# Kernel optimization log

Measured on AMD Instinct MI355X. Metric: run time of the kernel, lower is better.

## Reference

```python
import jax, jax.numpy as jnp
import numpy as np

B = 16384          # batch of graphs
N = 4              # nodes per graph (hardcoded in module)
F_IN = 4           # node features
F_E = 4            # edge features
CH = 128           # EdgeConditionedConv channels
HID = 256          # final Dense units (gnn hidden_dim)
OBS_DIM = 3 + N * F_IN + N * N + N * N * F_E  # 99


def _glorot(k, shape, fan):
    return jax.random.normal(k, shape, jnp.float32) * (1.0 / np.sqrt(fan))


def setup_inputs() -> dict:
    key = jax.random.key(0)
    ks = jax.random.split(key, 8)
    return {
        "observations": jax.random.normal(ks[0], (B, OBS_DIM), jnp.float32),
        # ECCConv filter-generating network: single Dense(F_E -> CH*F_IN)
        "W_fgn": _glorot(ks[1], (F_E, CH * F_IN), F_E),
        "b_fgn": jnp.zeros((CH * F_IN,), jnp.float32),
        # ECCConv root weight + bias
        "W_root": _glorot(ks[2], (F_IN, CH), F_IN),
        "b_conv": jnp.zeros((CH,), jnp.float32),
        # GlobalAttnSumPool attention vector
        "attn_kernel": _glorot(ks[3], (CH,), CH),
        # final Dense(tanh)
        "W_dense": _glorot(ks[4], (CH, HID), CH),
        "b_dense": jnp.zeros((HID,), jnp.float32),
    }


def reference(observations, W_fgn, b_fgn, W_root, b_conv, attn_kernel, W_dense, b_dense):
    Bn = observations.shape[0]
    obs = observations[:, 3:]
    X = obs[:, : N * F_IN].reshape(Bn, N, F_IN)                     # [B,N,F]
    A = obs[:, N * F_IN : N * F_IN + N * N].reshape(Bn, N, N)        # [B,N,N]
    E = obs[:, N * F_IN + N * N :].reshape(Bn, N, N, F_E)            # [B,N,N,Fe]

    # EdgeConditionedConv: per-edge filter generated from edge features,
    # reshaped to (B, N, N, CH, F_IN)  [channels-out first, as in spektral]
    K = (E @ W_fgn + b_fgn).reshape(Bn, N, N, CH, F_IN)
    # out[b,t,c] = sum_{s,f} A[b,t,s] * K[b,t,s,c,f] * X[b,s,f]  + root + bias
    msg = jnp.einsum('btscf,bts,bsf->btc', K, A, X)
    Xc = jax.nn.relu(msg + X @ W_root + b_conv)                      # [B,N,CH]

    # GlobalAttnSumPool: softmax over nodes of X @ a, weighted sum
    attn = jax.nn.softmax(jnp.einsum('bnc,c->bn', Xc, attn_kernel), axis=-1)
    pooled = jnp.einsum('bn,bnc->bc', attn, Xc)                      # [B,CH]

    return jnp.tanh(pooled @ W_dense + b_dense)                      # [B,HID]
```

## Files before the change

kernel.cpp:

```cpp
#include <hip/hip_runtime.h>

#define OBS_DIM 99
#define CH      128
#define HID     256
#define BPB     16

typedef short s8v __attribute__((ext_vector_type(8)));
typedef short s4v __attribute__((ext_vector_type(4)));
typedef float f4v __attribute__((ext_vector_type(4)));

__device__ __forceinline__ float ftanh(float x) {
    const float t = __expf(2.f * x);
    return 1.f - 2.f * __builtin_amdgcn_rcpf(t + 1.f);
}

__device__ __forceinline__ unsigned short f2bf(float f) {
    union { float f; unsigned u; } v; v.f = f;
    unsigned r = (v.u + 0x7fffu + ((v.u >> 16) & 1u)) >> 16;
    return (unsigned short)r;
}

__device__ __forceinline__ float bf2f(unsigned short u) {
    union { unsigned u; float f; } v; v.u = ((unsigned)u) << 16;
    return v.f;
}

__device__ __forceinline__ int kmap(int vb, int g, int j) {
    return vb ? (g * 4 + (j & 3) + 16 * (j >> 2)) : (g * 8 + j);
}

__device__ __forceinline__ float wbig_val(int k, int c, const float* Wf,
                                          const float* bf, const float* Wr,
                                          const float* bc) {
    if (k < 16) return Wf[(k >> 2) * 512 + c * 4 + (k & 3)];
    if (k < 20) return bf[c * 4 + (k - 16)];
    if (k < 24) return Wr[(k - 20) * CH + c];
    if (k == 24) return bc[c];
    return 0.f;
}

__global__ __launch_bounds__(256) void prepack(const float* __restrict__ W,
                                               const float* __restrict__ Wf,
                                               const float* __restrict__ bf,
                                               const float* __restrict__ Wr,
                                               const float* __restrict__ bc,
                                               unsigned short* __restrict__ ws) {
    const int gid = blockIdx.x * 256 + threadIdx.x;
    if (gid < 8192) {
        const int vb = gid >> 12, g = gid & 4095;
        const int tile = g >> 6, l = g & 63;
        const int kt = tile >> 4, nt = tile & 15;
        const int h = nt * 16 + (l & 15);
        unsigned short vh[8], vl[8];
        #pragma unroll
        for (int j = 0; j < 8; ++j) {
            const int k = kt * 32 + kmap(vb, l >> 4, j);
            const float wv = W[(size_t)k * HID + h];
            vh[j] = f2bf(wv);
            vl[j] = f2bf(wv - bf2f(vh[j]));
        }
        unsigned short* dh = ws + (size_t)vb * 65536 + (size_t)g * 8;
        *reinterpret_cast<s8v*>(dh)         = *reinterpret_cast<const s8v*>(vh);
        *reinterpret_cast<s8v*>(dh + 32768) = *reinterpret_cast<const s8v*>(vl);
    } else if (gid < 9216) {
        const int g2 = gid - 8192;
        const int vb = g2 >> 9, rest = g2 & 511;
        const int nt = rest >> 6, l = rest & 63;
        const int c = nt * 16 + (l & 15);
        unsigned short vh[8], vl[8];
        #pragma unroll
        for (int j = 0; j < 8; ++j) {
            const int k = kmap(vb, l >> 4, j);
            const float wv = wbig_val(k, c, Wf, bf, Wr, bc);
            vh[j] = f2bf(wv);
            vl[j] = f2bf(wv - bf2f(vh[j]));
        }
        unsigned short* dh = ws + 131072 + (size_t)vb * 8192 + (size_t)(nt * 64 + l) * 8;
        *reinterpret_cast<s8v*>(dh)        = *reinterpret_cast<const s8v*>(vh);
        *reinterpret_cast<s8v*>(dh + 4096) = *reinterpret_cast<const s8v*>(vl);
    }
}

template <int USE_MFMA>
__global__ __launch_bounds__(256, 3) void gnn_fused(
    const float* __restrict__ obs,
    const float* __restrict__ W_fgn,
    const float* __restrict__ b_fgn,
    const float* __restrict__ W_root,
    const float* __restrict__ b_conv,
    const float* __restrict__ attn_k,
    const float* __restrict__ W_dense,
    const unsigned short* __restrict__ wb,
    const float* __restrict__ b_dense,
    float* __restrict__ out)
{
    __shared__ __align__(16) unsigned char smem[43264];
    auto feat_h  = reinterpret_cast<unsigned short (*)[40]>(smem);
    auto feat_l  = reinterpret_cast<unsigned short (*)[40]>(smem + 5120);
    auto lobs    = reinterpret_cast<float (*)[96]>(smem + 10240);
    auto xcp     = reinterpret_cast<float (*)[129]>(smem + 10240);
    auto part    = reinterpret_cast<float (*)[64]>(smem + 5120);
    auto attnl   = reinterpret_cast<float*>(smem + 6144);
    auto lpool_h = reinterpret_cast<unsigned short (*)[136]>(smem);
    auto lpool_l = reinterpret_cast<unsigned short (*)[136]>(smem + 10240);

    const int tid  = threadIdx.x;
    const int b0   = blockIdx.x * BPB;
    const int lane = tid & 63;
    const int w    = tid >> 6;

    for (int i = tid; i < BPB * 96; i += 256) {
        const int bi = i / 96, col = i - bi * 96;
        lobs[bi][col] = obs[(size_t)(b0 + bi) * OBS_DIM + 3 + col];
    }

    int variant = 3;
    int bi_r[4] = {0, 0, 0, 0}, hx_r[4] = {0, 0, 0, 0};
    if (USE_MFMA) {
        s8v ac, ab2, lab, ones;
        #pragma unroll
        for (int j = 0; j < 8; ++j) {
            const int g = lane >> 4;
            ac[j]   = (short)f2bf((float)(kmap(0, g, j) + 1));
            ab2[j]  = (short)f2bf((float)(kmap(1, g, j) + 1));
            lab[j]  = (short)f2bf((float)(lane & 15));
            ones[j] = (short)0x3F80;
        }
        const f4v z = {0.f, 0.f, 0.f, 0.f};
        const f4v dcc = __builtin_amdgcn_mfma_f32_16x16x32_bf16(ac,  ac,  z, 0, 0, 0);
        const f4v dcb = __builtin_amdgcn_mfma_f32_16x16x32_bf16(ac,  ab2, z, 0, 0, 0);
        const f4v dbc = __builtin_amdgcn_mfma_f32_16x16x32_bf16(ab2, ac,  z, 0, 0, 0);
        const float EXP = 11440.f;
        if      (__all(dcc[0] == EXP)) variant = 0;
        else if (__all(dcb[0] == EXP)) variant = 1;
        else if (__all(dbc[0] == EXP)) variant = 2;

        const f4v rowv = __builtin_amdgcn_mfma_f32_16x16x32_bf16(lab, ones, z, 0, 0, 0);
        const f4v colv = __builtin_amdgcn_mfma_f32_16x16x32_bf16(ones, lab, z, 0, 0, 0);
        #pragma unroll
        for (int r = 0; r < 4; ++r) {
            int bv = (int)(rowv[r] * 0.03125f + 0.5f);
            int hv = (int)(colv[r] * 0.03125f + 0.5f);
            bi_r[r] = bv < 0 ? 0 : (bv > 15 ? 15 : bv);
            hx_r[r] = hv < 0 ? 0 : (hv > 15 ? 15 : hv);
        }
    }
    __syncthreads();

    {
        const int bi = tid >> 4, t = (tid >> 2) & 3, e = tid & 3;
        const int row = bi * 4 + t;
        float m[4] = {0.f, 0.f, 0.f, 0.f};
        #pragma unroll
        for (int s = 0; s < 4; ++s) {
            const float ae = lobs[bi][16 + t * 4 + s] * lobs[bi][32 + (t * 4 + s) * 4 + e];
            #pragma unroll
            for (int f = 0; f < 4; ++f) m[f] = fmaf(ae, lobs[bi][s * 4 + f], m[f]);
        }
        #pragma unroll
        for (int f = 0; f < 4; ++f) {
            const unsigned short h = f2bf(m[f]);
            feat_h[row][e * 4 + f] = h;
            feat_l[row][e * 4 + f] = f2bf(m[f] - bf2f(h));
        }
    }
    if (tid < 64) {
        const int bi = tid >> 2, t = tid & 3, row = bi * 4 + t;
        #pragma unroll
        for (int f = 0; f < 4; ++f) {
            float ax = 0.f;
            #pragma unroll
            for (int s = 0; s < 4; ++s)
                ax = fmaf(lobs[bi][16 + t * 4 + s], lobs[bi][s * 4 + f], ax);
            const unsigned short h = f2bf(ax);
            feat_h[row][16 + f] = h;
            feat_l[row][16 + f] = f2bf(ax - bf2f(h));
        }
    } else if (tid < 128) {
        const int q = tid - 64;
        const int bi = q >> 2, t = q & 3, row = bi * 4 + t;
        #pragma unroll
        for (int f = 0; f < 4; ++f) {
            const float xv = lobs[bi][t * 4 + f];
            const unsigned short h = f2bf(xv);
            feat_h[row][20 + f] = h;
            feat_l[row][20 + f] = f2bf(xv - bf2f(h));
        }
        feat_h[row][24] = 0x3F80; feat_l[row][24] = 0;
        #pragma unroll
        for (int k = 25; k < 32; ++k) { feat_h[row][k] = 0; feat_l[row][k] = 0; }
    }
    __syncthreads();

    if (variant < 3) {
        const s8v* B1h = reinterpret_cast<const s8v*>(wb + 131072 + (variant == 1 ? 8192 : 0));
        const s8v* B1l = B1h + 512;
        s8v bh[2], bl[2];
        #pragma unroll
        for (int ctl = 0; ctl < 2; ++ctl) {
            const int idx = (w * 2 + ctl) * 64 + lane;
            bh[ctl] = B1h[idx]; bl[ctl] = B1l[idx];
        }
        #pragma unroll
        for (int rt = 0; rt < 4; ++rt) {
            const int row = rt * 16 + (lane & 15);
            s8v ah, al;
            if (variant != 2) {
                ah = *reinterpret_cast<const s8v*>(&feat_h[row][(lane >> 4) * 8]);
                al = *reinterpret_cast<const s8v*>(&feat_l[row][(lane >> 4) * 8]);
            } else {
                const s4v h0 = *reinterpret_cast<const s4v*>(&feat_h[row][(lane >> 4) * 4]);
                const s4v h1 = *reinterpret_cast<const s4v*>(&feat_h[row][16 + (lane >> 4) * 4]);
                const s4v l0 = *reinterpret_cast<const s4v*>(&feat_l[row][(lane >> 4) * 4]);
                const s4v l1 = *reinterpret_cast<const s4v*>(&feat_l[row][16 + (lane >> 4) * 4]);
                ah = __builtin_shufflevector(h0, h1, 0, 1, 2, 3, 4, 5, 6, 7);
                al = __builtin_shufflevector(l0, l1, 0, 1, 2, 3, 4, 5, 6, 7);
            }
            #pragma unroll
            for (int ctl = 0; ctl < 2; ++ctl) {
                f4v acc = {0.f, 0.f, 0.f, 0.f};
                acc = __builtin_amdgcn_mfma_f32_16x16x32_bf16(al, bh[ctl], acc, 0, 0, 0);
                acc = __builtin_amdgcn_mfma_f32_16x16x32_bf16(ah, bl[ctl], acc, 0, 0, 0);
                acc = __builtin_amdgcn_mfma_f32_16x16x32_bf16(ah, bh[ctl], acc, 0, 0, 0);
                const int ct = w * 2 + ctl;
                #pragma unroll
                for (int r = 0; r < 4; ++r)
                    xcp[rt * 16 + bi_r[r]][ct * 16 + hx_r[r]] = fmaxf(acc[r], 0.f);
            }
        }
    } else {
        const int c = tid & 127, hf = tid >> 7;
        for (int r = hf * 32; r < hf * 32 + 32; ++r) {
            float s = 0.f;
            #pragma unroll 5
            for (int k = 0; k < 25; ++k)
                s = fmaf(bf2f(feat_h[r][k]) + bf2f(feat_l[r][k]),
                         wbig_val(k, c, W_fgn, b_fgn, W_root, b_conv), s);
            xcp[r][c] = fmaxf(s, 0.f);
        }
    }
    __syncthreads();

    {
        const int cb = w * 32;
        float p = 0.f;
        #pragma unroll 8
        for (int cc = 0; cc < 32; ++cc)
            p = fmaf(xcp[lane][cb + cc], attn_k[cb + cc], p);
        part[w][lane] = p;
    }
    __syncthreads();

    if (tid < 64) {
        const float l = part[0][tid] + part[1][tid] + part[2][tid] + part[3][tid];
        float m1 = fmaxf(l, __shfl_xor(l, 1, 64));
        m1 = fmaxf(m1, __shfl_xor(m1, 2, 64));
        const float e = __expf(l - m1);
        float s = e + __shfl_xor(e, 1, 64);
        s += __shfl_xor(s, 2, 64);
        attnl[tid] = e * __builtin_amdgcn_rcpf(s);
    }
    __syncthreads();

    {
        const int item = tid >> 4, cb = (tid & 15) * 8;
        float pl[8] = {0.f, 0.f, 0.f, 0.f, 0.f, 0.f, 0.f, 0.f};
        #pragma unroll
        for (int t = 0; t < 4; ++t) {
            const float a = attnl[item * 4 + t];
            #pragma unroll
            for (int j = 0; j < 8; ++j)
                pl[j] = fmaf(a, xcp[item * 4 + t][cb + j], pl[j]);
        }
        __syncthreads();
        #pragma unroll
        for (int j = 0; j < 8; ++j) {
            const unsigned short h = f2bf(pl[j]);
            lpool_h[item][cb + j] = h;
            lpool_l[item][cb + j] = f2bf(pl[j] - bf2f(h));
        }
    }
    __syncthreads();

    if (variant < 3) {
        const s8v* Bh = reinterpret_cast<const s8v*>(wb + (variant == 1 ? 65536 : 0));
        const s8v* Bl = reinterpret_cast<const s8v*>(wb + (variant == 1 ? 98304 : 32768));
        f4v acc[4] = {f4v{0,0,0,0}, f4v{0,0,0,0}, f4v{0,0,0,0}, f4v{0,0,0,0}};
        #pragma unroll
        for (int ks = 0; ks < 4; ++ks) {
            s8v ah, al;
            if (variant != 2) {
                ah = *reinterpret_cast<const s8v*>(&lpool_h[lane & 15][ks * 32 + (lane >> 4) * 8]);
                al = *reinterpret_cast<const s8v*>(&lpool_l[lane & 15][ks * 32 + (lane >> 4) * 8]);
            } else {
                const s4v h0 = *reinterpret_cast<const s4v*>(&lpool_h[lane & 15][ks * 32 + (lane >> 4) * 4]);
                const s4v h1 = *reinterpret_cast<const s4v*>(&lpool_h[lane & 15][ks * 32 + 16 + (lane >> 4) * 4]);
                const s4v l0 = *reinterpret_cast<const s4v*>(&lpool_l[lane & 15][ks * 32 + (lane >> 4) * 4]);
                const s4v l1 = *reinterpret_cast<const s4v*>(&lpool_l[lane & 15][ks * 32 + 16 + (lane >> 4) * 4]);
                ah = __builtin_shufflevector(h0, h1, 0, 1, 2, 3, 4, 5, 6, 7);
                al = __builtin_shufflevector(l0, l1, 0, 1, 2, 3, 4, 5, 6, 7);
            }
            #pragma unroll
            for (int nt = 0; nt < 4; ++nt) {
                const int idx = (ks * 16 + w * 4 + nt) * 64 + lane;
                const s8v bh = Bh[idx], bl = Bl[idx];
                acc[nt] = __builtin_amdgcn_mfma_f32_16x16x32_bf16(al, bh, acc[nt], 0, 0, 0);
                acc[nt] = __builtin_amdgcn_mfma_f32_16x16x32_bf16(ah, bl, acc[nt], 0, 0, 0);
                acc[nt] = __builtin_amdgcn_mfma_f32_16x16x32_bf16(ah, bh, acc[nt], 0, 0, 0);
            }
        }
        #pragma unroll
        for (int nt = 0; nt < 4; ++nt) {
            #pragma unroll
            for (int r = 0; r < 4; ++r) {
                const int h = w * 64 + nt * 16 + hx_r[r];
                out[(size_t)(b0 + bi_r[r]) * HID + h] = ftanh(acc[nt][r] + b_dense[h]);
            }
        }
    } else {
        const int col0 = w * 64 + (lane & 15) * 4;
        const int rb   = (lane >> 4) * 4;
        float acc[4][4];
        #pragma unroll
        for (int j = 0; j < 4; ++j)
            #pragma unroll
            for (int i = 0; i < 4; ++i) acc[j][i] = 0.f;
        for (int cc = 0; cc < CH; ++cc) {
            const float4 wr = *reinterpret_cast<const float4*>(&W_dense[(size_t)cc * HID + col0]);
            #pragma unroll
            for (int j = 0; j < 4; ++j) {
                const float p = bf2f(lpool_h[rb + j][cc]) + bf2f(lpool_l[rb + j][cc]);
                acc[j][0] = fmaf(p, wr.x, acc[j][0]);
                acc[j][1] = fmaf(p, wr.y, acc[j][1]);
                acc[j][2] = fmaf(p, wr.z, acc[j][2]);
                acc[j][3] = fmaf(p, wr.w, acc[j][3]);
            }
        }
        const float4 bd = *reinterpret_cast<const float4*>(&b_dense[col0]);
        #pragma unroll
        for (int j = 0; j < 4; ++j) {
            float4 o;
            o.x = ftanh(acc[j][0] + bd.x);
            o.y = ftanh(acc[j][1] + bd.y);
            o.z = ftanh(acc[j][2] + bd.z);
            o.w = ftanh(acc[j][3] + bd.w);
            *reinterpret_cast<float4*>(&out[(size_t)(b0 + rb + j) * HID + col0]) = o;
        }
    }
}

extern "C" void kernel_launch(void* const* d_in, const int* in_sizes, int n_in,
                              void* d_out, int out_size, void* d_ws, size_t ws_size,
                              hipStream_t stream) {
    const float* obs     = (const float*)d_in[0];
    const float* W_fgn   = (const float*)d_in[1];
    const float* b_fgn   = (const float*)d_in[2];
    const float* W_root  = (const float*)d_in[3];
    const float* b_conv  = (const float*)d_in[4];
    const float* attn_k  = (const float*)d_in[5];
    const float* W_dense = (const float*)d_in[6];
    const float* b_dense = (const float*)d_in[7];
    float* out = (float*)d_out;

    const int Bn = in_sizes[0] / OBS_DIM;
    const bool use_mfma = (ws_size >= 320 * 1024) && (d_ws != nullptr);

    if (use_mfma) {
        unsigned short* wb = (unsigned short*)d_ws;
        prepack<<<36, 256, 0, stream>>>(W_dense, W_fgn, b_fgn, W_root, b_conv, wb);
        gnn_fused<1><<<Bn / BPB, 256, 0, stream>>>(obs, W_fgn, b_fgn, W_root, b_conv,
                                                   attn_k, W_dense, wb, b_dense, out);
    } else {
        gnn_fused<0><<<Bn / BPB, 256, 0, stream>>>(obs, W_fgn, b_fgn, W_root, b_conv,
                                                   attn_k, W_dense, nullptr, b_dense, out);
    }
}
```

Baseline: 27.05 us.

## Keep conv outputs in registers, fuse attention pooling, hoist MFMA layout probe to prepack

The per-block MFMA layout and variant probe moves into the prepack kernel and is written once to workspace. The main kernel reads it from there. The ECC conv outputs now stay in registers, and attention logits are reduced with shuffles instead of through a 64x129 shared-memory tile. This shrinks shared memory from about 43KB to 19KB and raises launch bounds to 4 blocks per SM for more occupancy. The cost is more register pressure from holding xc, plus a dependency on the probe result in global memory.

```diff
diff --git a/kernel.cpp b/kernel.cpp
--- a/kernel.cpp
+++ b/kernel.cpp
@@ -79,10 +79,64 @@
         *reinterpret_cast<s8v*>(dh)        = *reinterpret_cast<const s8v*>(vh);
         *reinterpret_cast<s8v*>(dh + 4096) = *reinterpret_cast<const s8v*>(vl);
     }
-}
-
-template <int USE_MFMA>
-__global__ __launch_bounds__(256, 3) void gnn_fused(
+
+    if (blockIdx.x == 0 && threadIdx.x < 64) {
+        const int lane = threadIdx.x;
+        const int g = lane >> 4;
+        s8v ac, ab2, lab, ones;
+        #pragma unroll
+        for (int j = 0; j < 8; ++j) {
+            ac[j]   = (short)f2bf((float)(kmap(0, g, j) + 1));
+            ab2[j]  = (short)f2bf((float)(kmap(1, g, j) + 1));
+            lab[j]  = (short)f2bf((float)(lane & 15));
+            ones[j] = (short)0x3F80;
+        }
+        const f4v z = {0.f, 0.f, 0.f, 0.f};
+        const f4v dcc = __builtin_amdgcn_mfma_f32_16x16x32_bf16(ac,  ac,  z, 0, 0, 0);
+        const f4v dcb = __builtin_amdgcn_mfma_f32_16x16x32_bf16(ac,  ab2, z, 0, 0, 0);
+        const f4v dbc = __builtin_amdgcn_mfma_f32_16x16x32_bf16(ab2, ac,  z, 0, 0, 0);
+        const float EXP = 11440.f;
+        int variant = 3;
+        if      (__all(dcc[0] == EXP)) variant = 0;
+        else if (__all(dcb[0] == EXP)) variant = 1;
+        else if (__all(dbc[0] == EXP)) variant = 2;
+
+        const f4v rowv = __builtin_amdgcn_mfma_f32_16x16x32_bf16(lab, ones, z, 0, 0, 0);
+        const f4v colv = __builtin_amdgcn_mfma_f32_16x16x32_bf16(ones, lab, z, 0, 0, 0);
+        int bi[4], hx[4];
+        #pragma unroll
+        for (int r = 0; r < 4; ++r) {
+            int bv = (int)(rowv[r] * 0.03125f + 0.5f);
+            int hv = (int)(colv[r] * 0.03125f + 0.5f);
+            bi[r] = bv < 0 ? 0 : (bv > 15 ? 15 : bv);
+            hx[r] = hv < 0 ? 0 : (hv > 15 ? 15 : hv);
+        }
+        bool gb = (bi[0] >> 2 == bi[1] >> 2) && (bi[1] >> 2 == bi[2] >> 2) &&
+                  (bi[2] >> 2 == bi[3] >> 2);
+        gb = gb && (((1 << (bi[0] & 3)) | (1 << (bi[1] & 3)) |
+                     (1 << (bi[2] & 3)) | (1 << (bi[3] & 3))) == 0xF);
+        gb = gb && (hx[0] == hx[1]) && (hx[1] == hx[2]) && (hx[2] == hx[3]);
+        const int pk = bi[0] | (bi[1] << 4) | (bi[2] << 8) | (bi[3] << 12)
+                     | (hx[0] << 16) | (hx[1] << 20) | (hx[2] << 24) | (hx[3] << 28);
+        int bip = pk & 0xFFFF;
+        bool same = true;
+        #pragma unroll
+        for (int st = 1; st < 16; st <<= 1)
+            same = same && (bip == __shfl_xor(bip, st, 64));
+        unsigned mset = 1u << hx[0];
+        #pragma unroll
+        for (int st = 1; st < 16; st <<= 1)
+            mset |= (unsigned)__shfl_xor((int)mset, st, 64);
+        gb = gb && same && (mset == 0xFFFFu);
+        const int gb_all = __all(gb ? 1 : 0);
+
+        int* pr = reinterpret_cast<int*>(ws + 147456);
+        pr[lane] = pk;
+        if (lane == 0) pr[64] = variant | (gb_all ? 16 : 0);
+    }
+}
+
+__global__ __launch_bounds__(256, 4) void gnn_main(
     const float* __restrict__ obs,
     const float* __restrict__ W_fgn,
     const float* __restrict__ b_fgn,
@@ -91,59 +145,42 @@
     const float* __restrict__ attn_k,
     const float* __restrict__ W_dense,
     const unsigned short* __restrict__ wb,
+    const int* __restrict__ probe,
     const float* __restrict__ b_dense,
     float* __restrict__ out)
 {
-    __shared__ __align__(16) unsigned char smem[43264];
+    __shared__ __align__(16) unsigned char smem[18944];
     auto feat_h  = reinterpret_cast<unsigned short (*)[40]>(smem);
     auto feat_l  = reinterpret_cast<unsigned short (*)[40]>(smem + 5120);
+    auto part    = reinterpret_cast<float (*)[64]>(smem);
+    auto attnl   = reinterpret_cast<float*>(smem + 1024);
     auto lobs    = reinterpret_cast<float (*)[96]>(smem + 10240);
-    auto xcp     = reinterpret_cast<float (*)[129]>(smem + 10240);
-    auto part    = reinterpret_cast<float (*)[64]>(smem + 5120);
-    auto attnl   = reinterpret_cast<float*>(smem + 6144);
-    auto lpool_h = reinterpret_cast<unsigned short (*)[136]>(smem);
-    auto lpool_l = reinterpret_cast<unsigned short (*)[136]>(smem + 10240);
+    auto lpool_h = reinterpret_cast<unsigned short (*)[136]>(smem + 10240);
+    auto lpool_l = reinterpret_cast<unsigned short (*)[136]>(smem + 14592);
+    auto poolf   = reinterpret_cast<float (*)[136]>(smem + 10240);
 
     const int tid  = threadIdx.x;
     const int b0   = blockIdx.x * BPB;
     const int lane = tid & 63;
     const int w    = tid >> 6;
 
+    int variant = 3, groupable = 0;
+    int bi_r[4] = {0, 0, 0, 0}, hx_r[4] = {0, 0, 0, 0};
+    if (probe) {
+        const int pk   = probe[lane];
+        const int meta = probe[64];
+        variant   = meta & 7;
+        groupable = (meta >> 4) & 1;
+        #pragma unroll
+        for (int r = 0; r < 4; ++r) {
+            bi_r[r] = (pk >> (4 * r)) & 15;
+            hx_r[r] = (pk >> (16 + 4 * r)) & 15;
+        }
+    }
+
     for (int i = tid; i < BPB * 96; i += 256) {
         const int bi = i / 96, col = i - bi * 96;
         lobs[bi][col] = obs[(size_t)(b0 + bi) * OBS_DIM + 3 + col];
-    }
-
-    int variant = 3;
-    int bi_r[4] = {0, 0, 0, 0}, hx_r[4] = {0, 0, 0, 0};
-    if (USE_MFMA) {
-        s8v ac, ab2, lab, ones;
-        #pragma unroll
-        for (int j = 0; j < 8; ++j) {
-            const int g = lane >> 4;
-            ac[j]   = (short)f2bf((float)(kmap(0, g, j) + 1));
-            ab2[j]  = (short)f2bf((float)(kmap(1, g, j) + 1));
-            lab[j]  = (short)f2bf((float)(lane & 15));
-            ones[j] = (short)0x3F80;
-        }
-        const f4v z = {0.f, 0.f, 0.f, 0.f};
-        const f4v dcc = __builtin_amdgcn_mfma_f32_16x16x32_bf16(ac,  ac,  z, 0, 0, 0);
-        const f4v dcb = __builtin_amdgcn_mfma_f32_16x16x32_bf16(ac,  ab2, z, 0, 0, 0);
-        const f4v dbc = __builtin_amdgcn_mfma_f32_16x16x32_bf16(ab2, ac,  z, 0, 0, 0);
-        const float EXP = 11440.f;
-        if      (__all(dcc[0] == EXP)) variant = 0;
-        else if (__all(dcb[0] == EXP)) variant = 1;
-        else if (__all(dbc[0] == EXP)) variant = 2;
-
-        const f4v rowv = __builtin_amdgcn_mfma_f32_16x16x32_bf16(lab, ones, z, 0, 0, 0);
-        const f4v colv = __builtin_amdgcn_mfma_f32_16x16x32_bf16(ones, lab, z, 0, 0, 0);
-        #pragma unroll
-        for (int r = 0; r < 4; ++r) {
-            int bv = (int)(rowv[r] * 0.03125f + 0.5f);
-            int hv = (int)(colv[r] * 0.03125f + 0.5f);
-            bi_r[r] = bv < 0 ? 0 : (bv > 15 ? 15 : bv);
-            hx_r[r] = hv < 0 ? 0 : (hv > 15 ? 15 : hv);
-        }
     }
     __syncthreads();
 
@@ -192,15 +229,26 @@
     }
     __syncthreads();
 
-    if (variant < 3) {
+    if (variant < 3 && groupable) {
+        const int hx0 = hx_r[0];
+        const int ib  = bi_r[0] >> 2;
+
         const s8v* B1h = reinterpret_cast<const s8v*>(wb + 131072 + (variant == 1 ? 8192 : 0));
         const s8v* B1l = B1h + 512;
-        s8v bh[2], bl[2];
+        s8v bh1[2], bl1[2];
+        float akv[2];
         #pragma unroll
         for (int ctl = 0; ctl < 2; ++ctl) {
             const int idx = (w * 2 + ctl) * 64 + lane;
-            bh[ctl] = B1h[idx]; bl[ctl] = B1l[idx];
-        }
+            bh1[ctl] = B1h[idx]; bl1[ctl] = B1l[idx];
+            akv[ctl] = attn_k[w * 32 + ctl * 16 + hx0];
+        }
+
+        float xc[4][2][4];
+        float part16[16];
+        #pragma unroll
+        for (int i = 0; i < 16; ++i) part16[i] = 0.f;
+
         #pragma unroll
         for (int rt = 0; rt < 4; ++rt) {
             const int row = rt * 16 + (lane & 15);
@@ -219,73 +267,65 @@
             #pragma unroll
             for (int ctl = 0; ctl < 2; ++ctl) {
                 f4v acc = {0.f, 0.f, 0.f, 0.f};
-                acc = __builtin_amdgcn_mfma_f32_16x16x32_bf16(al, bh[ctl], acc, 0, 0, 0);
-                acc = __builtin_amdgcn_mfma_f32_16x16x32_bf16(ah, bl[ctl], acc, 0, 0, 0);
-                acc = __builtin_amdgcn_mfma_f32_16x16x32_bf16(ah, bh[ctl], acc, 0, 0, 0);
-                const int ct = w * 2 + ctl;
+                acc = __builtin_amdgcn_mfma_f32_16x16x32_bf16(al, bh1[ctl], acc, 0, 0, 0);
+                acc = __builtin_amdgcn_mfma_f32_16x16x32_bf16(ah, bl1[ctl], acc, 0, 0, 0);
+                acc = __builtin_amdgcn_mfma_f32_16x16x32_bf16(ah, bh1[ctl], acc, 0, 0, 0);
+                #pragma unroll
+                for (int r = 0; r < 4; ++r) {
+                    const float v = fmaxf(acc[r], 0.f);
+                    xc[rt][ctl][r] = v;
+                    part16[rt * 4 + r] = fmaf(v, akv[ctl], part16[rt * 4 + r]);
+                }
+            }
+        }
+
+        #pragma unroll
+        for (int st = 1; st < 16; st <<= 1) {
+            #pragma unroll
+            for (int i = 0; i < 16; ++i)
+                part16[i] += __shfl_xor(part16[i], st, 64);
+        }
+        __syncthreads();
+        if ((lane & 15) == 0) {
+            #pragma unroll
+            for (int rt = 0; rt < 4; ++rt)
                 #pragma unroll
                 for (int r = 0; r < 4; ++r)
-                    xcp[rt * 16 + bi_r[r]][ct * 16 + hx_r[r]] = fmaxf(acc[r], 0.f);
-            }
-        }
-    } else {
-        const int c = tid & 127, hf = tid >> 7;
-        for (int r = hf * 32; r < hf * 32 + 32; ++r) {
-            float s = 0.f;
-            #pragma unroll 5
-            for (int k = 0; k < 25; ++k)
-                s = fmaf(bf2f(feat_h[r][k]) + bf2f(feat_l[r][k]),
-                         wbig_val(k, c, W_fgn, b_fgn, W_root, b_conv), s);
-            xcp[r][c] = fmaxf(s, 0.f);
-        }
-    }
-    __syncthreads();
-
-    {
-        const int cb = w * 32;
-        float p = 0.f;
-        #pragma unroll 8
-        for (int cc = 0; cc < 32; ++cc)
-            p = fmaf(xcp[lane][cb + cc], attn_k[cb + cc], p);
-        part[w][lane] = p;
-    }
-    __syncthreads();
-
-    if (tid < 64) {
-        const float l = part[0][tid] + part[1][tid] + part[2][tid] + part[3][tid];
-        float m1 = fmaxf(l, __shfl_xor(l, 1, 64));
-        m1 = fmaxf(m1, __shfl_xor(m1, 2, 64));
-        const float e = __expf(l - m1);
-        float s = e + __shfl_xor(e, 1, 64);
-        s += __shfl_xor(s, 2, 64);
-        attnl[tid] = e * __builtin_amdgcn_rcpf(s);
-    }
-    __syncthreads();
-
-    {
-        const int item = tid >> 4, cb = (tid & 15) * 8;
-        float pl[8] = {0.f, 0.f, 0.f, 0.f, 0.f, 0.f, 0.f, 0.f};
-        #pragma unroll
-        for (int t = 0; t < 4; ++t) {
-            const float a = attnl[item * 4 + t];
-            #pragma unroll
-            for (int j = 0; j < 8; ++j)
-                pl[j] = fmaf(a, xcp[item * 4 + t][cb + j], pl[j]);
+                    part[w][rt * 16 + bi_r[r]] = part16[rt * 4 + r];
         }
         __syncthreads();
-        #pragma unroll
-        for (int j = 0; j < 8; ++j) {
-            const unsigned short h = f2bf(pl[j]);
-            lpool_h[item][cb + j] = h;
-            lpool_l[item][cb + j] = f2bf(pl[j] - bf2f(h));
-        }
-    }
-    __syncthreads();
-
-    if (variant < 3) {
+
+        if (tid < 64) {
+            const float l = part[0][tid] + part[1][tid] + part[2][tid] + part[3][tid];
+            float m1 = fmaxf(l, __shfl_xor(l, 1, 64));
+            m1 = fmaxf(m1, __shfl_xor(m1, 2, 64));
+            const float e = __expf(l - m1);
+            float s = e + __shfl_xor(e, 1, 64);
+            s += __shfl_xor(s, 2, 64);
+            attnl[tid] = e * __builtin_amdgcn_rcpf(s);
+        }
+        __syncthreads();
+
+        #pragma unroll
+        for (int rt = 0; rt < 4; ++rt) {
+            float p0 = 0.f, p1 = 0.f;
+            #pragma unroll
+            for (int r = 0; r < 4; ++r) {
+                const float a = attnl[rt * 16 + bi_r[r]];
+                p0 = fmaf(a, xc[rt][0][r], p0);
+                p1 = fmaf(a, xc[rt][1][r], p1);
+            }
+            const int item = rt * 4 + ib;
+            const int c0 = w * 32 + hx0, c1 = c0 + 16;
+            const unsigned short h0 = f2bf(p0), h1 = f2bf(p1);
+            lpool_h[item][c0] = h0;  lpool_l[item][c0] = f2bf(p0 - bf2f(h0));
+            lpool_h[item][c1] = h1;  lpool_l[item][c1] = f2bf(p1 - bf2f(h1));
+        }
+        __syncthreads();
+
         const s8v* Bh = reinterpret_cast<const s8v*>(wb + (variant == 1 ? 65536 : 0));
         const s8v* Bl = reinterpret_cast<const s8v*>(wb + (variant == 1 ? 98304 : 32768));
-        f4v acc[4] = {f4v{0,0,0,0}, f4v{0,0,0,0}, f4v{0,0,0,0}, f4v{0,0,0,0}};
+        f4v acc2[4] = {f4v{0,0,0,0}, f4v{0,0,0,0}, f4v{0,0,0,0}, f4v{0,0,0,0}};
         #pragma unroll
         for (int ks = 0; ks < 4; ++ks) {
             s8v ah, al;
@@ -304,9 +344,9 @@
             for (int nt = 0; nt < 4; ++nt) {
                 const int idx = (ks * 16 + w * 4 + nt) * 64 + lane;
                 const s8v bh = Bh[idx], bl = Bl[idx];
-                acc[nt] = __builtin_amdgcn_mfma_f32_16x16x32_bf16(al, bh, acc[nt], 0, 0, 0);
-                acc[nt] = __builtin_amdgcn_mfma_f32_16x16x32_bf16(ah, bl, acc[nt], 0, 0, 0);
-                acc[nt] = __builtin_amdgcn_mfma_f32_16x16x32_bf16(ah, bh, acc[nt], 0, 0, 0);
+                acc2[nt] = __builtin_amdgcn_mfma_f32_16x16x32_bf16(al, bh, acc2[nt], 0, 0, 0);
+                acc2[nt] = __builtin_amdgcn_mfma_f32_16x16x32_bf16(ah, bl, acc2[nt], 0, 0, 0);
+                acc2[nt] = __builtin_amdgcn_mfma_f32_16x16x32_bf16(ah, bh, acc2[nt], 0, 0, 0);
             }
         }
         #pragma unroll
@@ -314,10 +354,44 @@
             #pragma unroll
             for (int r = 0; r < 4; ++r) {
                 const int h = w * 64 + nt * 16 + hx_r[r];
-                out[(size_t)(b0 + bi_r[r]) * HID + h] = ftanh(acc[nt][r] + b_dense[h]);
+                out[(size_t)(b0 + bi_r[r]) * HID + h] = ftanh(acc2[nt][r] + b_dense[h]);
             }
         }
     } else {
+        #pragma unroll 1
+        for (int p = 0; p < 4; ++p) {
+            const int item = w * 4 + p;
+            float xc2[2][4], pt[4] = {0.f, 0.f, 0.f, 0.f};
+            #pragma unroll 1
+            for (int ch = 0; ch < 2; ++ch) {
+                const int cc = lane + ch * 64;
+                #pragma unroll
+                for (int t = 0; t < 4; ++t) {
+                    const int row = item * 4 + t;
+                    float v = 0.f;
+                    #pragma unroll 5
+                    for (int k = 0; k < 25; ++k) {
+                        const float fv = bf2f(feat_h[row][k]) + bf2f(feat_l[row][k]);
+                        v = fmaf(fv, wbig_val(k, cc, W_fgn, b_fgn, W_root, b_conv), v);
+                    }
+                    xc2[ch][t] = fmaxf(v, 0.f);
+                    pt[t] = fmaf(xc2[ch][t], attn_k[cc], pt[t]);
+                }
+            }
+            #pragma unroll
+            for (int st = 1; st < 64; st <<= 1) {
+                #pragma unroll
+                for (int t = 0; t < 4; ++t) pt[t] += __shfl_xor(pt[t], st, 64);
+            }
+            const float mx = fmaxf(fmaxf(pt[0], pt[1]), fmaxf(pt[2], pt[3]));
+            const float e0 = __expf(pt[0] - mx), e1 = __expf(pt[1] - mx);
+            const float e2 = __expf(pt[2] - mx), e3 = __expf(pt[3] - mx);
+            const float inv = 1.f / (e0 + e1 + e2 + e3);
+            poolf[item][lane]      = (e0 * xc2[0][0] + e1 * xc2[0][1] + e2 * xc2[0][2] + e3 * xc2[0][3]) * inv;
+            poolf[item][lane + 64] = (e0 * xc2[1][0] + e1 * xc2[1][1] + e2 * xc2[1][2] + e3 * xc2[1][3]) * inv;
+        }
+        __syncthreads();
+
         const int col0 = w * 64 + (lane & 15) * 4;
         const int rb   = (lane >> 4) * 4;
         float acc[4][4];
@@ -325,15 +399,27 @@
         for (int j = 0; j < 4; ++j)
             #pragma unroll
             for (int i = 0; i < 4; ++i) acc[j][i] = 0.f;
-        for (int cc = 0; cc < CH; ++cc) {
-            const float4 wr = *reinterpret_cast<const float4*>(&W_dense[(size_t)cc * HID + col0]);
+        #pragma unroll 4
+        for (int cc = 0; cc < CH; cc += 4) {
+            float4 pv[4], wr[4];
             #pragma unroll
             for (int j = 0; j < 4; ++j) {
-                const float p = bf2f(lpool_h[rb + j][cc]) + bf2f(lpool_l[rb + j][cc]);
-                acc[j][0] = fmaf(p, wr.x, acc[j][0]);
-                acc[j][1] = fmaf(p, wr.y, acc[j][1]);
-                acc[j][2] = fmaf(p, wr.z, acc[j][2]);
-                acc[j][3] = fmaf(p, wr.w, acc[j][3]);
+                pv[j].x = poolf[rb + j][cc];     pv[j].y = poolf[rb + j][cc + 1];
+                pv[j].z = poolf[rb + j][cc + 2]; pv[j].w = poolf[rb + j][cc + 3];
+            }
+            #pragma unroll
+            for (int k = 0; k < 4; ++k)
+                wr[k] = *reinterpret_cast<const float4*>(&W_dense[(size_t)(cc + k) * HID + col0]);
+            #pragma unroll
+            for (int j = 0; j < 4; ++j) {
+                const float pj[4] = {pv[j].x, pv[j].y, pv[j].z, pv[j].w};
+                #pragma unroll
+                for (int k = 0; k < 4; ++k) {
+                    acc[j][0] = fmaf(pj[k], wr[k].x, acc[j][0]);
+                    acc[j][1] = fmaf(pj[k], wr[k].y, acc[j][1]);
+                    acc[j][2] = fmaf(pj[k], wr[k].z, acc[j][2]);
+                    acc[j][3] = fmaf(pj[k], wr[k].w, acc[j][3]);
+                }
             }
         }
         const float4 bd = *reinterpret_cast<const float4*>(&b_dense[col0]);
@@ -363,15 +449,17 @@
     float* out = (float*)d_out;
 
     const int Bn = in_sizes[0] / OBS_DIM;
-    const bool use_mfma = (ws_size >= 320 * 1024) && (d_ws != nullptr);
-
-    if (use_mfma) {
+    const bool use_ws = (ws_size >= 320 * 1024) && (d_ws != nullptr);
+
+    if (use_ws) {
         unsigned short* wb = (unsigned short*)d_ws;
         prepack<<<36, 256, 0, stream>>>(W_dense, W_fgn, b_fgn, W_root, b_conv, wb);
-        gnn_fused<1><<<Bn / BPB, 256, 0, stream>>>(obs, W_fgn, b_fgn, W_root, b_conv,
-                                                   attn_k, W_dense, wb, b_dense, out);
+        gnn_main<<<Bn / BPB, 256, 0, stream>>>(obs, W_fgn, b_fgn, W_root, b_conv,
+                                               attn_k, W_dense, wb,
+                                               (const int*)(wb + 147456), b_dense, out);
     } else {
-        gnn_fused<0><<<Bn / BPB, 256, 0, stream>>>(obs, W_fgn, b_fgn, W_root, b_conv,
-                                                   attn_k, W_dense, nullptr, b_dense, out);
-    }
-}
+        gnn_main<<<Bn / BPB, 256, 0, stream>>>(obs, W_fgn, b_fgn, W_root, b_conv,
+                                               attn_k, W_dense, nullptr, nullptr,
+                                               b_dense, out);
+    }
+}
```

After: 24.81 us. -8.3%, faster.
